# Performance work log

Hardware: AMD Instinct MI355X
Metric: run time of the kernel (lower is better)

## Reference

```python
import jax, jax.numpy as jnp
import numpy as np

B, T, D, R = 16, 4096, 512, 256

# Buffers (match torch: linspace(0,T-1,R).long() truncates toward zero)
_LANDMARKS = np.linspace(0.0, T - 1, R).astype(np.int64)
_POS = np.arange(T)[:, None]                                   # [T,1]
_MASK = (_LANDMARKS[None, :] < _POS)                           # [T,R] bool: landmark j < position i
_TDIST = np.clip((_POS.astype(np.float32) - _LANDMARKS[None, :].astype(np.float32)) / T, 0.0, None).astype(np.float32)  # [T,R]


def setup_inputs() -> dict:
    key = jax.random.key(0)
    k1, k2, k3 = jax.random.split(key, 3)
    return {
        "z": jax.random.normal(k1, (B, T, D), dtype=jnp.float32),
        "gegenbauer_weights": jax.random.normal(k2, (3,), dtype=jnp.float32),
        "temporal_alpha": jax.random.normal(k3, (1,), dtype=jnp.float32),
    }


def reference(z, gegenbauer_weights, temporal_alpha):
    dtype = z.dtype
    mask = jnp.asarray(_MASK)                       # [T,R]
    tdist = jnp.asarray(_TDIST, dtype=dtype)        # [T,R]
    lm = jnp.asarray(_LANDMARKS)                    # [R]

    # F.normalize(z, dim=-1) with eps=1e-12
    norm = jnp.linalg.norm(z, axis=-1, keepdims=True)
    Q = z / jnp.maximum(norm, 1e-12)                # [B,T,D]
    K = Q[:, lm, :]                                 # [B,R,D]
    C = jnp.einsum('btd,brd->btr', Q, K)            # [B,T,R] cosine similarity

    # Gegenbauer mixture
    alpha = jax.nn.softmax(gegenbauer_weights)
    C2 = C * C
    P1 = (1.0 + C) * 0.5
    P2 = (3.0 * C2 - 1.0) * 0.5
    P3 = (5.0 * C2 * C - 3.0 * C) * 0.5
    Phi = alpha[0] * P1 + alpha[1] * P2 + alpha[2] * P3

    # Causal mask
    Phi = Phi * mask.astype(dtype)[None, :, :]

    # Temporal decay
    a_td = jax.nn.softplus(temporal_alpha[0])
    Phi = Phi * jnp.exp(-a_td * tdist)[None, :, :]

    # Row-sum normalization
    row_sum = jnp.maximum(Phi.sum(axis=-1, keepdims=True), 1e-6)
    Phi = Phi / row_sum

    # Append constant-ones feature -> [B,T,R+1]
    ones = jnp.ones((Phi.shape[0], Phi.shape[1], 1), dtype=dtype)
    return jnp.concatenate([Phi, ones], axis=-1)
```

## Files before the change

kernel.cpp:

```cpp
#include <hip/hip_runtime.h>
#include <hip/hip_bf16.h>
#include <math.h>

#define B_DIM 16
#define T_DIM 4096
#define D_DIM 512
#define R_DIM 256

#define TM 128
#define BK 64
#define LDP 72
#define NKS (D_DIM/32)

typedef __bf16 bf16x8 __attribute__((ext_vector_type(8)));
typedef float floatx4 __attribute__((ext_vector_type(4)));

__device__ __forceinline__ int landmark_of(int r) {
    if (r >= 255) return 4095;
    const double step = 4095.0 / 255.0;
    return (int)((double)r * step);
}

__device__ __forceinline__ void split_bf16(float x, __bf16& h, __bf16& l) {
    h = (__bf16)x;
    l = (__bf16)(x - (float)h);
}

__global__ void nystrom_prep_kernel(const float* __restrict__ z,
                                    __bf16* __restrict__ Khi, __bf16* __restrict__ Klo) {
    int blk = blockIdx.x;
    int b = blk >> 8;
    int r = blk & 255;
    int lane = threadIdx.x;
    int lm = landmark_of(r);
    const float* src = z + ((size_t)b * T_DIM + lm) * D_DIM + lane * 8;
    float4 v0 = ((const float4*)src)[0];
    float4 v1 = ((const float4*)src)[1];
    float ss = v0.x*v0.x + v0.y*v0.y + v0.z*v0.z + v0.w*v0.w
             + v1.x*v1.x + v1.y*v1.y + v1.z*v1.z + v1.w*v1.w;
    #pragma unroll
    for (int off = 1; off < 64; off <<= 1) ss += __shfl_xor(ss, off, 64);
    float inv = 1.0f / fmaxf(sqrtf(ss), 1e-12f);
    float q[8] = {v0.x*inv, v0.y*inv, v0.z*inv, v0.w*inv,
                  v1.x*inv, v1.y*inv, v1.z*inv, v1.w*inv};
    bf16x8 oh, ol;
    #pragma unroll
    for (int j = 0; j < 8; j++) { __bf16 h, l; split_bf16(q[j], h, l); oh[j] = h; ol[j] = l; }
    size_t dst = ((((size_t)b * NKS + (lane >> 2)) * 16 + (r >> 4)) * 64
                  + (size_t)(lane & 3) * 16 + (r & 15)) * 8;
    *(bf16x8*)(Khi + dst) = oh;
    *(bf16x8*)(Klo + dst) = ol;
}

__global__ __launch_bounds__(256, 2)
void nystrom_main_kernel(const float* __restrict__ z,
                         const __bf16* __restrict__ Khi, const __bf16* __restrict__ Klo,
                         const float* __restrict__ gw, const float* __restrict__ ta,
                         float* __restrict__ out) {
    __shared__ __attribute__((aligned(16))) char smem[36864];
    __shared__ int   lmtab[R_DIM];
    __shared__ float elmtab[R_DIM];

    __bf16* Ash = (__bf16*)(smem);
    __bf16* Asl = (__bf16*)(smem + 18432);
    float* red    = (float*)(smem);
    float* rnormp = (float*)(smem + 1024);
    float* rinvp  = (float*)(smem + 1536);
    float* rspart = (float*)(smem + 2048);

    const int tid  = threadIdx.x;
    const int b    = blockIdx.y;
    const int t0   = blockIdx.x * TM;
    const int lane = tid & 63;
    const int wv   = tid >> 6;
    const int quad = lane >> 4;
    const int ln   = lane & 15;

    float g0 = gw[0], g1 = gw[1], g2 = gw[2];
    float gm = fmaxf(g0, fmaxf(g1, g2));
    float e0 = expf(g0 - gm), e1 = expf(g1 - gm), e2 = expf(g2 - gm);
    float esum = e0 + e1 + e2;
    float al0 = e0 / esum, al1 = e1 / esum, al2 = e2 / esum;
    float ax = ta[0];
    float a_td = (ax > 20.f) ? ax : log1pf(expf(ax));

    {
        int lm = landmark_of(tid);
        lmtab[tid] = lm;
        elmtab[tid] = expf(a_td * (float)lm * (1.0f / 4096.0f));
    }

    const int srowA = tid >> 1;
    const int scolA = (tid & 1) * 32;
    const float* zrow = z + ((size_t)b * T_DIM + (t0 + srowA)) * D_DIM + scolA;

    const size_t kfoff = (size_t)b * (NKS * 16 * 64 * 8)
                       + (size_t)wv * 2048 + (size_t)lane * 8;
    const __bf16* khb = Khi + kfoff;
    const __bf16* klb = Klo + kfoff;

    floatx4 acc[8][4];
    #pragma unroll
    for (int i = 0; i < 8; i++)
        #pragma unroll
        for (int j = 0; j < 4; j++) acc[i][j] = (floatx4){0.f, 0.f, 0.f, 0.f};
    float ssq = 0.0f;

    float4 a0, a1, a2, a3, a4, a5, a6, a7;
    {
        const float4* ap = (const float4*)(zrow);
        a0 = ap[0]; a1 = ap[1]; a2 = ap[2]; a3 = ap[3];
        a4 = ap[4]; a5 = ap[5]; a6 = ap[6]; a7 = ap[7];
    }

    #pragma unroll 1
    for (int kt = 0; kt < D_DIM; kt += BK) {
        float av[32] = {a0.x,a0.y,a0.z,a0.w, a1.x,a1.y,a1.z,a1.w,
                        a2.x,a2.y,a2.z,a2.w, a3.x,a3.y,a3.z,a3.w,
                        a4.x,a4.y,a4.z,a4.w, a5.x,a5.y,a5.z,a5.w,
                        a6.x,a6.y,a6.z,a6.w, a7.x,a7.y,a7.z,a7.w};
        #pragma unroll
        for (int j = 0; j < 32; j++) ssq += av[j] * av[j];
        #pragma unroll
        for (int g = 0; g < 4; g++) {
            bf16x8 ph, pl;
            #pragma unroll
            for (int j = 0; j < 8; j++) {
                __bf16 h, l; split_bf16(av[g*8+j], h, l); ph[j] = h; pl[j] = l;
            }
            *(bf16x8*)&Ash[srowA * LDP + scolA + g*8] = ph;
            *(bf16x8*)&Asl[srowA * LDP + scolA + g*8] = pl;
        }
        __syncthreads();

        if (kt + BK < D_DIM) {
            const float4* ap = (const float4*)(zrow + kt + BK);
            a0 = ap[0]; a1 = ap[1]; a2 = ap[2]; a3 = ap[3];
            a4 = ap[4]; a5 = ap[5]; a6 = ap[6]; a7 = ap[7];
        }

        const int ksb = kt >> 5;
        #pragma unroll
        for (int s = 0; s < 2; s++) {
            const __bf16* khp = khb + (size_t)(ksb + s) * 8192;
            const __bf16* klp = klb + (size_t)(ksb + s) * 8192;
            bf16x8 bh[4], bl[4];
            #pragma unroll
            for (int ni = 0; ni < 4; ni++) {
                bh[ni] = *(const bf16x8*)(khp + ni * 512);
                bl[ni] = *(const bf16x8*)(klp + ni * 512);
            }
            const int koff = s * 32 + quad * 8;
            #pragma unroll
            for (int mi = 0; mi < 8; mi++) {
                bf16x8 afh = *(const bf16x8*)&Ash[(mi * 16 + ln) * LDP + koff];
                bf16x8 afl = *(const bf16x8*)&Asl[(mi * 16 + ln) * LDP + koff];
                #pragma unroll
                for (int ni = 0; ni < 4; ni++) {
                    acc[mi][ni] = __builtin_amdgcn_mfma_f32_16x16x32_bf16(
                        afh, bh[ni], acc[mi][ni], 0, 0, 0);
                    acc[mi][ni] = __builtin_amdgcn_mfma_f32_16x16x32_bf16(
                        afh, bl[ni], acc[mi][ni], 0, 0, 0);
                    acc[mi][ni] = __builtin_amdgcn_mfma_f32_16x16x32_bf16(
                        afl, bh[ni], acc[mi][ni], 0, 0, 0);
                }
            }
        }
        __syncthreads();
    }

    red[tid] = ssq;
    __syncthreads();
    if (tid < TM) {
        float s = red[tid * 2] + red[tid * 2 + 1];
        rnormp[tid] = 1.0f / fmaxf(sqrtf(s), 1e-12f);
    }
    __syncthreads();

    int   lm_r[4];
    float elm_r[4];
    #pragma unroll
    for (int ni = 0; ni < 4; ni++) {
        int r = wv * 64 + ni * 16 + ln;
        lm_r[ni]  = lmtab[r];
        elm_r[ni] = elmtab[r];
    }

    #pragma unroll
    for (int mi = 0; mi < 8; mi++) {
        #pragma unroll
        for (int reg = 0; reg < 4; reg++) {
            int row = mi * 16 + quad * 4 + reg;
            int t = t0 + row;
            float rn = rnormp[row];
            float e_t = expf(-a_td * (float)t * (1.0f / 4096.0f));
            float s = 0.f;
            #pragma unroll
            for (int ni = 0; ni < 4; ni++) {
                float phi = 0.f;
                if (lm_r[ni] < t) {
                    float c  = acc[mi][ni][reg] * rn;
                    float c2 = c * c;
                    float P1 = 0.5f * (1.f + c);
                    float P2 = 0.5f * (3.f * c2 - 1.f);
                    float P3 = 0.5f * (5.f * c2 * c - 3.f * c);
                    float p  = al0 * P1 + al1 * P2 + al2 * P3;
                    phi = p * e_t * elm_r[ni];
                }
                acc[mi][ni][reg] = phi;
                s += phi;
            }
            #pragma unroll
            for (int off = 1; off < 16; off <<= 1) s += __shfl_xor(s, off, 64);
            if (ln == 0) rspart[wv * TM + row] = s;
        }
    }
    __syncthreads();
    if (tid < TM) {
        float rs = rspart[0 * TM + tid] + rspart[1 * TM + tid]
                 + rspart[2 * TM + tid] + rspart[3 * TM + tid];
        rinvp[tid] = 1.0f / fmaxf(rs, 1e-6f);
    }
    __syncthreads();

    float* ob = out + ((size_t)b * T_DIM + t0) * 257;
    #pragma unroll
    for (int mi = 0; mi < 8; mi++) {
        #pragma unroll
        for (int reg = 0; reg < 4; reg++) {
            int row = mi * 16 + quad * 4 + reg;
            float inv = rinvp[row];
            #pragma unroll
            for (int ni = 0; ni < 4; ni++) {
                int r = wv * 64 + ni * 16 + ln;
                ob[(size_t)row * 257 + r] = acc[mi][ni][reg] * inv;
            }
        }
    }
    if (tid < TM) ob[(size_t)tid * 257 + 256] = 1.0f;
}

extern "C" void kernel_launch(void* const* d_in, const int* in_sizes, int n_in,
                              void* d_out, int out_size, void* d_ws, size_t ws_size,
                              hipStream_t stream) {
    const float* z  = (const float*)d_in[0];
    const float* gw = (const float*)d_in[1];
    const float* ta = (const float*)d_in[2];
    float* out = (float*)d_out;
    __bf16* Khi = (__bf16*)d_ws;
    __bf16* Klo = (__bf16*)((char*)d_ws + (size_t)B_DIM * R_DIM * D_DIM * 2);

    nystrom_prep_kernel<<<dim3(B_DIM * R_DIM), 64, 0, stream>>>(z, Khi, Klo);
    nystrom_main_kernel<<<dim3(T_DIM / TM, B_DIM), 256, 0, stream>>>(z, Khi, Klo, gw, ta, out);
}
```

Measured before the change: 270.1 us.

## Halve row tile to 64 and double-buffer the A tile in LDS

Cuts the row tile from 128 to 64, which shrinks the accumulator array and raises the occupancy target to 3 blocks per CU. It also double-buffers the split bf16 hi/lo A tile in shared memory, so the next slice is converted and written while MFMAs consume the current one, leaving one barrier per k step. The aim is better latency hiding and twice as many blocks for the grid. The cost is twice as many reloads of the K fragments per output row, since each block now covers fewer rows.

```diff
diff --git a/kernel.cpp b/kernel.cpp
--- a/kernel.cpp
+++ b/kernel.cpp
@@ -7,7 +7,7 @@
 #define D_DIM 512
 #define R_DIM 256
 
-#define TM 128
+#define TM 64
 #define BK 64
 #define LDP 72
 #define NKS (D_DIM/32)
@@ -52,7 +52,7 @@
     *(bf16x8*)(Klo + dst) = ol;
 }
 
-__global__ __launch_bounds__(256, 2)
+__global__ __launch_bounds__(256, 3)
 void nystrom_main_kernel(const float* __restrict__ z,
                          const __bf16* __restrict__ Khi, const __bf16* __restrict__ Klo,
                          const float* __restrict__ gw, const float* __restrict__ ta,
@@ -61,12 +61,10 @@
     __shared__ int   lmtab[R_DIM];
     __shared__ float elmtab[R_DIM];
 
-    __bf16* Ash = (__bf16*)(smem);
-    __bf16* Asl = (__bf16*)(smem + 18432);
     float* red    = (float*)(smem);
     float* rnormp = (float*)(smem + 1024);
-    float* rinvp  = (float*)(smem + 1536);
-    float* rspart = (float*)(smem + 2048);
+    float* rinvp  = (float*)(smem + 1280);
+    float* rspart = (float*)(smem + 1536);
 
     const int tid  = threadIdx.x;
     const int b    = blockIdx.y;
@@ -90,8 +88,8 @@
         elmtab[tid] = expf(a_td * (float)lm * (1.0f / 4096.0f));
     }
 
-    const int srowA = tid >> 1;
-    const int scolA = (tid & 1) * 32;
+    const int srowA = tid >> 2;
+    const int scolA = (tid & 3) * 16;
     const float* zrow = z + ((size_t)b * T_DIM + (t0 + srowA)) * D_DIM + scolA;
 
     const size_t kfoff = (size_t)b * (NKS * 16 * 64 * 8)
@@ -99,46 +97,49 @@
     const __bf16* khb = Khi + kfoff;
     const __bf16* klb = Klo + kfoff;
 
-    floatx4 acc[8][4];
-    #pragma unroll
-    for (int i = 0; i < 8; i++)
+    floatx4 acc[4][4];
+    #pragma unroll
+    for (int i = 0; i < 4; i++)
         #pragma unroll
         for (int j = 0; j < 4; j++) acc[i][j] = (floatx4){0.f, 0.f, 0.f, 0.f};
     float ssq = 0.0f;
 
-    float4 a0, a1, a2, a3, a4, a5, a6, a7;
+    float4 a0, a1, a2, a3;
+
     {
         const float4* ap = (const float4*)(zrow);
         a0 = ap[0]; a1 = ap[1]; a2 = ap[2]; a3 = ap[3];
-        a4 = ap[4]; a5 = ap[5]; a6 = ap[6]; a7 = ap[7];
-    }
+        float av[16] = {a0.x,a0.y,a0.z,a0.w, a1.x,a1.y,a1.z,a1.w,
+                        a2.x,a2.y,a2.z,a2.w, a3.x,a3.y,a3.z,a3.w};
+        #pragma unroll
+        for (int j = 0; j < 16; j++) ssq += av[j] * av[j];
+        __bf16* wsh = (__bf16*)(smem);
+        __bf16* wsl = (__bf16*)(smem + 9216);
+        #pragma unroll
+        for (int g = 0; g < 2; g++) {
+            bf16x8 ph, pl;
+            #pragma unroll
+            for (int j = 0; j < 8; j++) {
+                __bf16 h, l; split_bf16(av[g*8+j], h, l); ph[j] = h; pl[j] = l;
+            }
+            *(bf16x8*)&wsh[srowA * LDP + scolA + g*8] = ph;
+            *(bf16x8*)&wsl[srowA * LDP + scolA + g*8] = pl;
+        }
+    }
+    __syncthreads();
 
     #pragma unroll 1
     for (int kt = 0; kt < D_DIM; kt += BK) {
-        float av[32] = {a0.x,a0.y,a0.z,a0.w, a1.x,a1.y,a1.z,a1.w,
-                        a2.x,a2.y,a2.z,a2.w, a3.x,a3.y,a3.z,a3.w,
-                        a4.x,a4.y,a4.z,a4.w, a5.x,a5.y,a5.z,a5.w,
-                        a6.x,a6.y,a6.z,a6.w, a7.x,a7.y,a7.z,a7.w};
-        #pragma unroll
-        for (int j = 0; j < 32; j++) ssq += av[j] * av[j];
-        #pragma unroll
-        for (int g = 0; g < 4; g++) {
-            bf16x8 ph, pl;
-            #pragma unroll
-            for (int j = 0; j < 8; j++) {
-                __bf16 h, l; split_bf16(av[g*8+j], h, l); ph[j] = h; pl[j] = l;
-            }
-            *(bf16x8*)&Ash[srowA * LDP + scolA + g*8] = ph;
-            *(bf16x8*)&Asl[srowA * LDP + scolA + g*8] = pl;
-        }
-        __syncthreads();
-
-        if (kt + BK < D_DIM) {
+        const int cur = (kt >> 6) & 1;
+        const bool has_next = (kt + BK < D_DIM);
+
+        if (has_next) {
             const float4* ap = (const float4*)(zrow + kt + BK);
             a0 = ap[0]; a1 = ap[1]; a2 = ap[2]; a3 = ap[3];
-            a4 = ap[4]; a5 = ap[5]; a6 = ap[6]; a7 = ap[7];
-        }
-
+        }
+
+        const __bf16* Ash = (const __bf16*)(smem + cur * 18432);
+        const __bf16* Asl = (const __bf16*)(smem + cur * 18432 + 9216);
         const int ksb = kt >> 5;
         #pragma unroll
         for (int s = 0; s < 2; s++) {
@@ -152,7 +153,7 @@
             }
             const int koff = s * 32 + quad * 8;
             #pragma unroll
-            for (int mi = 0; mi < 8; mi++) {
+            for (int mi = 0; mi < 4; mi++) {
                 bf16x8 afh = *(const bf16x8*)&Ash[(mi * 16 + ln) * LDP + koff];
                 bf16x8 afl = *(const bf16x8*)&Asl[(mi * 16 + ln) * LDP + koff];
                 #pragma unroll
@@ -166,13 +167,32 @@
                 }
             }
         }
+
+        if (has_next) {
+            float av[16] = {a0.x,a0.y,a0.z,a0.w, a1.x,a1.y,a1.z,a1.w,
+                            a2.x,a2.y,a2.z,a2.w, a3.x,a3.y,a3.z,a3.w};
+            #pragma unroll
+            for (int j = 0; j < 16; j++) ssq += av[j] * av[j];
+            __bf16* wsh = (__bf16*)(smem + (cur ^ 1) * 18432);
+            __bf16* wsl = (__bf16*)(smem + (cur ^ 1) * 18432 + 9216);
+            #pragma unroll
+            for (int g = 0; g < 2; g++) {
+                bf16x8 ph, pl;
+                #pragma unroll
+                for (int j = 0; j < 8; j++) {
+                    __bf16 h, l; split_bf16(av[g*8+j], h, l); ph[j] = h; pl[j] = l;
+                }
+                *(bf16x8*)&wsh[srowA * LDP + scolA + g*8] = ph;
+                *(bf16x8*)&wsl[srowA * LDP + scolA + g*8] = pl;
+            }
+        }
         __syncthreads();
     }
 
     red[tid] = ssq;
     __syncthreads();
     if (tid < TM) {
-        float s = red[tid * 2] + red[tid * 2 + 1];
+        float s = red[tid * 4] + red[tid * 4 + 1] + red[tid * 4 + 2] + red[tid * 4 + 3];
         rnormp[tid] = 1.0f / fmaxf(sqrtf(s), 1e-12f);
     }
     __syncthreads();
@@ -187,7 +207,7 @@
     }
 
     #pragma unroll
-    for (int mi = 0; mi < 8; mi++) {
+    for (int mi = 0; mi < 4; mi++) {
         #pragma unroll
         for (int reg = 0; reg < 4; reg++) {
             int row = mi * 16 + quad * 4 + reg;
@@ -225,7 +245,7 @@
 
     float* ob = out + ((size_t)b * T_DIM + t0) * 257;
     #pragma unroll
-    for (int mi = 0; mi < 8; mi++) {
+    for (int mi = 0; mi < 4; mi++) {
         #pragma unroll
         for (int reg = 0; reg < 4; reg++) {
             int row = mi * 16 + quad * 4 + reg;
```

Result: faster. 259.6 us (-3.9%).
